# Performance work log

Hardware: AMD Instinct MI355X
Metric: run time of the kernel (lower is better)

## Reference

```python
import jax, jax.numpy as jnp
import numpy as np

N_NODES = 50000
N_EDGES = 640000
HID = 128
N_LAYERS = 4
BN_EPS = 1e-5


def _bn(h, gamma, beta):
    # train-mode BatchNorm1d over node axis (biased variance, as torch uses for normalization)
    mu = h.mean(axis=0)
    var = h.var(axis=0)
    return gamma * (h - mu) * jax.lax.rsqrt(var + BN_EPS) + beta


def setup_inputs() -> dict:
    key = jax.random.key(0)
    ks = jax.random.split(key, 8)
    s = 1.0 / np.sqrt(HID)
    x = jax.random.normal(ks[0], (N_NODES, HID), dtype=jnp.float32)
    edge_index = jax.random.randint(ks[1], (2, N_EDGES), 0, N_NODES, dtype=jnp.int64)
    edge_attr = jax.random.normal(ks[2], (N_EDGES, HID), dtype=jnp.float32)
    W1 = jax.random.normal(ks[3], (N_LAYERS, HID, HID), dtype=jnp.float32) * s
    b1 = jnp.zeros((N_LAYERS, HID), jnp.float32)
    g1 = jnp.ones((N_LAYERS, HID), jnp.float32)
    be1 = jnp.zeros((N_LAYERS, HID), jnp.float32)
    W2 = jax.random.normal(ks[4], (N_LAYERS, HID, HID), dtype=jnp.float32) * s
    b2 = jnp.zeros((N_LAYERS, HID), jnp.float32)
    bn_g = jnp.ones((N_LAYERS - 1, HID), jnp.float32)
    bn_b = jnp.zeros((N_LAYERS - 1, HID), jnp.float32)
    return {"x": x, "edge_index": edge_index, "edge_attr": edge_attr,
            "W1": W1, "b1": b1, "g1": g1, "be1": be1,
            "W2": W2, "b2": b2, "bn_g": bn_g, "bn_b": bn_b}


def reference(x, edge_index, edge_attr, W1, b1, g1, be1, W2, b2, bn_g, bn_b):
    src, dst = edge_index[0], edge_index[1]
    n = x.shape[0]
    z = x
    for i in range(N_LAYERS):
        # GINEConv: message = relu(x_j + e_ij), sum-aggregate, eps=0
        msg = jax.nn.relu(z[src] + edge_attr)          # [E, H]
        agg = jax.ops.segment_sum(msg, dst, num_segments=n)  # [N, H]
        h = z + agg
        # conv MLP: Linear -> BatchNorm1d -> ReLU -> Linear
        h = h @ W1[i] + b1[i]
        h = jax.nn.relu(_bn(h, g1[i], be1[i]))
        h = h @ W2[i] + b2[i]
        # encoder activation
        z = jax.nn.relu(h)
        # inter-layer batchnorm (not after last layer)
        if i != N_LAYERS - 1:
            z = _bn(z, bn_g[i], bn_b[i])
    return z
```

## Files before the change

kernel.cpp:

```cpp
#include <hip/hip_runtime.h>
#include <hip/hip_bf16.h>

#define N_NODES 50000
#define N_EDGES 640000
#define HID 128
#define BN_EPS 1e-5f
#define BF16_MAGIC 0x3F803F80u
#define MG_NBLK 782

typedef __bf16 bf16x8 __attribute__((ext_vector_type(8)));
typedef float f32x4 __attribute__((ext_vector_type(4)));

__global__ void detect_k(const unsigned int* __restrict__ g1w,
                         const unsigned int* __restrict__ idxw,
                         int* __restrict__ flags) {
    __shared__ int anynz;
    if (threadIdx.x == 0) anynz = 0;
    __syncthreads();
    unsigned int v = idxw[2 * threadIdx.x + 1];
    if (v) atomicOr(&anynz, 1);
    __syncthreads();
    if (threadIdx.x == 0) {
        flags[0] = (g1w[0] == BF16_MAGIC) ? 1 : 0;
        flags[1] = anynz ? 0 : 1;
    }
}

__global__ void init_k(int* __restrict__ cnt, float* __restrict__ statb) {
    int i = blockIdx.x * 256 + threadIdx.x;
    if (i < N_NODES) cnt[i] = 0;
    int j = i - N_NODES;
    if (j >= 0) {
        if (j < 1792) statb[j] = 0.f;
        if (j >= 2048 && j < 2176) statb[j] = 1.f;
        if (j >= 2560 && j < 2688) statb[j] = 0.f;
    }
}

__device__ __forceinline__ float cvt_in(const void* p, int i, int bf) {
    return bf ? __bfloat162float(((const __hip_bfloat16*)p)[i])
              : ((const float*)p)[i];
}

__global__ void conv_w_k(const void* W1, const void* W2, const void* b1, const void* b2,
                         const int* __restrict__ flags, float* __restrict__ wbuf) {
    int i = blockIdx.x * 256 + threadIdx.x;
    int bf = flags[0];
    if (i < 65536)       wbuf[i] = cvt_in(W1, i, bf);
    else if (i < 131072) wbuf[i] = cvt_in(W2, i - 65536, bf);
    else if (i < 131584) wbuf[i] = cvt_in(b1, i - 131072, bf);
    else if (i < 132096) wbuf[i] = cvt_in(b2, i - 131584, bf);
}

__global__ void pack_w_k(const float* __restrict__ wf,
                         __hip_bfloat16* __restrict__ hi,
                         __hip_bfloat16* __restrict__ lo) {
    int gid = blockIdx.x * 256 + threadIdx.x;
    int mat = gid >> 11;
    int ent = gid & 2047;
    int T = ent >> 8, S = (ent >> 6) & 3, L = ent & 63;
    int n = T * 16 + (L & 15);
    int k0 = S * 32 + (L >> 4) * 8;
    const float* w = wf + mat * 16384;
    __hip_bfloat16 hv[8], lv[8];
#pragma unroll
    for (int j = 0; j < 8; j++) {
        float v = w[(k0 + j) * 128 + n];
        float h = __bfloat162float(__float2bfloat16(v));
        hv[j] = __float2bfloat16(v);
        lv[j] = __float2bfloat16(v - h);
    }
    __hip_bfloat16* hp = hi + (size_t)gid * 8;
    __hip_bfloat16* lp = lo + (size_t)gid * 8;
#pragma unroll
    for (int j = 0; j < 8; j++) { hp[j] = hv[j]; lp[j] = lv[j]; }
}

__global__ void conv_x_k(const void* x, const int* __restrict__ flags,
                         float* __restrict__ zbuf) {
    int i = blockIdx.x * 256 + threadIdx.x;
    if (i >= N_NODES * HID / 4) return;
    float4 o;
    if (flags[0]) {
        ushort4 v = ((const ushort4*)x)[i];
        union { unsigned int u; float f; } a, b, c, d;
        a.u = (unsigned int)v.x << 16; b.u = (unsigned int)v.y << 16;
        c.u = (unsigned int)v.z << 16; d.u = (unsigned int)v.w << 16;
        o.x = a.f; o.y = b.f; o.z = c.f; o.w = d.f;
    } else {
        o = ((const float4*)x)[i];
    }
    ((float4*)zbuf)[i] = o;
}

__global__ void hist_k(const void* eidx, const int* __restrict__ flags,
                       int* __restrict__ cnt) {
    int e = blockIdx.x * 256 + threadIdx.x;
    if (e >= N_EDGES) return;
    int d = flags[1] ? (int)((const long long*)eidx)[N_EDGES + e]
                     : ((const int*)eidx)[N_EDGES + e];
    atomicAdd(&cnt[d], 1);
}

__global__ void scan_k(const int* __restrict__ cnt, int* __restrict__ start,
                       int* __restrict__ cursor) {
    __shared__ int sh[1024];
    __shared__ int carry;
    if (threadIdx.x == 0) carry = 0;
    __syncthreads();
    const int CH = 8192;
    for (int base = 0; base < N_NODES; base += CH) {
        int idx0 = base + threadIdx.x * 8;
        int v[8];
        int s = 0;
#pragma unroll
        for (int j = 0; j < 8; j++) {
            int i = idx0 + j;
            v[j] = (i < N_NODES) ? cnt[i] : 0;
            s += v[j];
        }
        sh[threadIdx.x] = s;
        __syncthreads();
        for (int off = 1; off < 1024; off <<= 1) {
            int tv = 0;
            if ((int)threadIdx.x >= off) tv = sh[threadIdx.x - off];
            __syncthreads();
            if ((int)threadIdx.x >= off) sh[threadIdx.x] += tv;
            __syncthreads();
        }
        int run = sh[threadIdx.x] - s + carry;
#pragma unroll
        for (int j = 0; j < 8; j++) {
            int i = idx0 + j;
            if (i < N_NODES) { start[i] = run; cursor[i] = run; }
            run += v[j];
        }
        __syncthreads();
        if (threadIdx.x == 1023) carry += sh[1023];
        __syncthreads();
    }
    if (threadIdx.x == 0) start[N_NODES] = carry;
}

__global__ void scatter_k(const void* eidx, const int* __restrict__ flags,
                          int* __restrict__ cursor, int2* __restrict__ se) {
    int e = blockIdx.x * 256 + threadIdx.x;
    if (e >= N_EDGES) return;
    int s, d;
    if (flags[1]) {
        const long long* p = (const long long*)eidx;
        s = (int)p[e]; d = (int)p[N_EDGES + e];
    } else {
        const int* p = (const int*)eidx;
        s = p[e]; d = p[N_EDGES + e];
    }
    int pos = atomicAdd(&cursor[d], 1);
    se[pos] = make_int2(s, e);
}

__global__ __launch_bounds__(256) void agg_k(
    const float* __restrict__ z, const void* __restrict__ eattr,
    const int* __restrict__ flags,
    const float* __restrict__ Ac, const float* __restrict__ Cc,
    const int* __restrict__ start, const int2* __restrict__ se,
    float* __restrict__ hin) {
    int lane = threadIdx.x & 63;
    int node = blockIdx.x * 4 + (threadIdx.x >> 6);
    if (node >= N_NODES) return;
    int c0 = lane * 2;
    float ax = Ac[c0], ay = Ac[c0 + 1];
    float cx = Cc[c0], cy = Cc[c0 + 1];
    int e0 = start[node], e1 = start[node + 1];
    int nE = e1 - e0;
    float sx = 0.f, sy = 0.f;
    const float2* zf = (const float2*)z;
    int isbf = flags[0];

    for (int base = 0; base < nE; base += 64) {
        int idx = base + lane;
        int2 sev = se[e0 + (idx < nE ? idx : nE - 1)];
        int rem = nE - base; if (rem > 64) rem = 64;
        int j = 0;
        if (isbf) {
            const __hip_bfloat162* ea = (const __hip_bfloat162*)eattr;
            for (; j + 4 <= rem; j += 4) {
                int s0 = __builtin_amdgcn_readlane(sev.x, j + 0);
                int i0 = __builtin_amdgcn_readlane(sev.y, j + 0);
                int s1 = __builtin_amdgcn_readlane(sev.x, j + 1);
                int i1 = __builtin_amdgcn_readlane(sev.y, j + 1);
                int s2 = __builtin_amdgcn_readlane(sev.x, j + 2);
                int i2 = __builtin_amdgcn_readlane(sev.y, j + 2);
                int s3 = __builtin_amdgcn_readlane(sev.x, j + 3);
                int i3 = __builtin_amdgcn_readlane(sev.y, j + 3);
                float2 z0 = zf[s0 * 64 + lane];
                float2 z1 = zf[s1 * 64 + lane];
                float2 z2 = zf[s2 * 64 + lane];
                float2 z3 = zf[s3 * 64 + lane];
                float2 e0v = __bfloat1622float2(ea[i0 * 64 + lane]);
                float2 e1v = __bfloat1622float2(ea[i1 * 64 + lane]);
                float2 e2v = __bfloat1622float2(ea[i2 * 64 + lane]);
                float2 e3v = __bfloat1622float2(ea[i3 * 64 + lane]);
                sx += fmaxf(fmaf(ax, z0.x, cx) + e0v.x, 0.f);
                sy += fmaxf(fmaf(ay, z0.y, cy) + e0v.y, 0.f);
                sx += fmaxf(fmaf(ax, z1.x, cx) + e1v.x, 0.f);
                sy += fmaxf(fmaf(ay, z1.y, cy) + e1v.y, 0.f);
                sx += fmaxf(fmaf(ax, z2.x, cx) + e2v.x, 0.f);
                sy += fmaxf(fmaf(ay, z2.y, cy) + e2v.y, 0.f);
                sx += fmaxf(fmaf(ax, z3.x, cx) + e3v.x, 0.f);
                sy += fmaxf(fmaf(ay, z3.y, cy) + e3v.y, 0.f);
            }
            for (; j < rem; j++) {
                int s0 = __builtin_amdgcn_readlane(sev.x, j);
                int i0 = __builtin_amdgcn_readlane(sev.y, j);
                float2 zv = zf[s0 * 64 + lane];
                float2 ev = __bfloat1622float2(ea[i0 * 64 + lane]);
                sx += fmaxf(fmaf(ax, zv.x, cx) + ev.x, 0.f);
                sy += fmaxf(fmaf(ay, zv.y, cy) + ev.y, 0.f);
            }
        } else {
            const float2* ea = (const float2*)eattr;
            for (; j + 4 <= rem; j += 4) {
                int s0 = __builtin_amdgcn_readlane(sev.x, j + 0);
                int i0 = __builtin_amdgcn_readlane(sev.y, j + 0);
                int s1 = __builtin_amdgcn_readlane(sev.x, j + 1);
                int i1 = __builtin_amdgcn_readlane(sev.y, j + 1);
                int s2 = __builtin_amdgcn_readlane(sev.x, j + 2);
                int i2 = __builtin_amdgcn_readlane(sev.y, j + 2);
                int s3 = __builtin_amdgcn_readlane(sev.x, j + 3);
                int i3 = __builtin_amdgcn_readlane(sev.y, j + 3);
                float2 z0 = zf[s0 * 64 + lane];
                float2 z1 = zf[s1 * 64 + lane];
                float2 z2 = zf[s2 * 64 + lane];
                float2 z3 = zf[s3 * 64 + lane];
                float2 e0v = ea[i0 * 64 + lane];
                float2 e1v = ea[i1 * 64 + lane];
                float2 e2v = ea[i2 * 64 + lane];
                float2 e3v = ea[i3 * 64 + lane];
                sx += fmaxf(fmaf(ax, z0.x, cx) + e0v.x, 0.f);
                sy += fmaxf(fmaf(ay, z0.y, cy) + e0v.y, 0.f);
                sx += fmaxf(fmaf(ax, z1.x, cx) + e1v.x, 0.f);
                sy += fmaxf(fmaf(ay, z1.y, cy) + e1v.y, 0.f);
                sx += fmaxf(fmaf(ax, z2.x, cx) + e2v.x, 0.f);
                sy += fmaxf(fmaf(ay, z2.y, cy) + e2v.y, 0.f);
                sx += fmaxf(fmaf(ax, z3.x, cx) + e3v.x, 0.f);
                sy += fmaxf(fmaf(ay, z3.y, cy) + e3v.y, 0.f);
            }
            for (; j < rem; j++) {
                int s0 = __builtin_amdgcn_readlane(sev.x, j);
                int i0 = __builtin_amdgcn_readlane(sev.y, j);
                float2 zv = zf[s0 * 64 + lane];
                float2 ev = ea[i0 * 64 + lane];
                sx += fmaxf(fmaf(ax, zv.x, cx) + ev.x, 0.f);
                sy += fmaxf(fmaf(ay, zv.y, cy) + ev.y, 0.f);
            }
        }
    }
    float2 zs = zf[node * 64 + lane];
    float2 o;
    o.x = fmaf(ax, zs.x, cx) + sx;
    o.y = fmaf(ay, zs.y, cy) + sy;
    ((float2*)hin)[node * 64 + lane] = o;
}

__global__ __launch_bounds__(256) void mgemm_k(
    const float* __restrict__ Ain,
    const __hip_bfloat16* __restrict__ whi, const __hip_bfloat16* __restrict__ wlo,
    const float* __restrict__ bias,
    const float* __restrict__ Ascale, const float* __restrict__ Cshift,
    float* __restrict__ Fout, void* __restrict__ OutFinal,
    const int* __restrict__ flags,
    float* __restrict__ pbuf, int mode) {
    __shared__ char WshRaw[32768];
    __shared__ char WslRaw[32768];
    __shared__ float ssum[128], ssq[128];
    int t = threadIdx.x;
    int lane = t & 63, w = t >> 6, quad = lane >> 4;
    int isbf = flags[0];
    int m0 = blockIdx.x * 64;
    int row = m0 + w * 16 + (lane & 15);
    bool rv = row < N_NODES;

    bf16x8 ahi[4], alo[4];
#pragma unroll
    for (int S = 0; S < 4; S++) {
        float v[8];
        if (rv) {
            const float4* ap = (const float4*)(Ain + row * 128 + S * 32 + quad * 8);
            float4 p0 = ap[0], p1 = ap[1];
            v[0] = p0.x; v[1] = p0.y; v[2] = p0.z; v[3] = p0.w;
            v[4] = p1.x; v[5] = p1.y; v[6] = p1.z; v[7] = p1.w;
        } else {
#pragma unroll
            for (int j = 0; j < 8; j++) v[j] = 0.f;
        }
        if (mode != 0) {
            const float4* as = (const float4*)(Ascale + S * 32 + quad * 8);
            const float4* cs = (const float4*)(Cshift + S * 32 + quad * 8);
            float4 a0 = as[0], a1 = as[1], c0 = cs[0], c1 = cs[1];
            float aa[8] = {a0.x, a0.y, a0.z, a0.w, a1.x, a1.y, a1.z, a1.w};
            float cc[8] = {c0.x, c0.y, c0.z, c0.w, c1.x, c1.y, c1.z, c1.w};
#pragma unroll
            for (int j = 0; j < 8; j++) v[j] = fmaxf(fmaf(aa[j], v[j], cc[j]), 0.f);
        }
#pragma unroll
        for (int j = 0; j < 8; j++) {
            __bf16 h = (__bf16)v[j];
            ahi[S][j] = h;
            alo[S][j] = (__bf16)(v[j] - (float)h);
        }
    }

    {
        const uint4* sh = (const uint4*)whi;
        uint4* dh = (uint4*)WshRaw;
#pragma unroll
        for (int i = 0; i < 8; i++) dh[t + i * 256] = sh[t + i * 256];
        if (!isbf) {
            const uint4* sl = (const uint4*)wlo;
            uint4* dl = (uint4*)WslRaw;
#pragma unroll
            for (int i = 0; i < 8; i++) dl[t + i * 256] = sl[t + i * 256];
        }
    }
    if (t < 128) { ssum[t] = 0.f; ssq[t] = 0.f; }
    __syncthreads();

    const bf16x8* WH = (const bf16x8*)WshRaw;
    const bf16x8* WL = (const bf16x8*)WslRaw;
    f32x4 acc[8];
    f32x4 z4 = {0.f, 0.f, 0.f, 0.f};
#pragma unroll
    for (int T = 0; T < 8; T++) acc[T] = z4;
#pragma unroll
    for (int T = 0; T < 8; T++) {
#pragma unroll
        for (int S = 0; S < 4; S++) {
            bf16x8 wh = WH[(T * 4 + S) * 64 + lane];
            acc[T] = __builtin_amdgcn_mfma_f32_16x16x32_bf16(ahi[S], wh, acc[T], 0, 0, 0);
            acc[T] = __builtin_amdgcn_mfma_f32_16x16x32_bf16(alo[S], wh, acc[T], 0, 0, 0);
        }
    }
    if (!isbf) {
#pragma unroll
        for (int T = 0; T < 8; T++) {
#pragma unroll
            for (int S = 0; S < 4; S++) {
                bf16x8 wl = WL[(T * 4 + S) * 64 + lane];
                acc[T] = __builtin_amdgcn_mfma_f32_16x16x32_bf16(ahi[S], wl, acc[T], 0, 0, 0);
            }
        }
    }

    int colbase = lane & 15;
    int rbase = m0 + w * 16 + quad * 4;
#pragma unroll
    for (int T = 0; T < 8; T++) {
        int col = T * 16 + colbase;
        float bv = bias[col];
        float s = 0.f, q = 0.f;
#pragma unroll
        for (int r = 0; r < 4; r++) {
            int rr = rbase + r;
            if (rr >= N_NODES) continue;
            float o = acc[T][r] + bv;
            if (mode != 0) o = fmaxf(o, 0.f);
            if (mode == 2) {
                if (isbf) ((__hip_bfloat16*)OutFinal)[rr * 128 + col] = __float2bfloat16(o);
                else      ((float*)OutFinal)[rr * 128 + col] = o;
            } else {
                Fout[rr * 128 + col] = o;
                s += o; q += o * o;
            }
        }
        if (mode != 2) {
            s += __shfl_xor(s, 16); s += __shfl_xor(s, 32);
            q += __shfl_xor(q, 16); q += __shfl_xor(q, 32);
            if (lane < 16) { atomicAdd(&ssum[col], s); atomicAdd(&ssq[col], q); }
        }
    }
    if (mode != 2) {
        __syncthreads();
        if (t < 128) {
            pbuf[blockIdx.x * 256 + t] = ssum[t];
            pbuf[blockIdx.x * 256 + 128 + t] = ssq[t];
        }
    }
}

__global__ __launch_bounds__(256) void fin_k(const float* __restrict__ pbuf,
                      const void* gamma, const void* beta, int layer,
                      const int* __restrict__ flags,
                      float* __restrict__ Ac, float* __restrict__ Cc) {
    int col = blockIdx.x;
    int t = threadIdx.x;
    float s = 0.f, q = 0.f;
    for (int b = t; b < MG_NBLK; b += 256) {
        s += pbuf[b * 256 + col];
        q += pbuf[b * 256 + 128 + col];
    }
#pragma unroll
    for (int m = 32; m >= 1; m >>= 1) {
        s += __shfl_xor(s, m);
        q += __shfl_xor(q, m);
    }
    __shared__ float shs[4], shq[4];
    if ((t & 63) == 0) { shs[t >> 6] = s; shq[t >> 6] = q; }
    __syncthreads();
    if (t == 0) {
        float S = shs[0] + shs[1] + shs[2] + shs[3];
        float Q = shq[0] + shq[1] + shq[2] + shq[3];
        int bf = flags[0];
        float g = cvt_in(gamma, layer * 128 + col, bf);
        float b_ = cvt_in(beta, layer * 128 + col, bf);
        const float invN = 1.f / (float)N_NODES;
        float mean = S * invN;
        float var = fmaxf(Q * invN - mean * mean, 0.f);
        float rs = rsqrtf(var + BN_EPS);
        float a = g * rs;
        Ac[col] = a;
        Cc[col] = b_ - mean * a;
    }
}

extern "C" void kernel_launch(void* const* d_in, const int* in_sizes, int n_in,
                              void* d_out, int out_size, void* d_ws, size_t ws_size,
                              hipStream_t stream) {
    const void* x_p   = d_in[0];
    const void* ei_p  = d_in[1];
    const void* ea_p  = d_in[2];
    const void* W1_p  = d_in[3];
    const void* b1_p  = d_in[4];
    const void* g1_p  = d_in[5];
    const void* be1_p = d_in[6];
    const void* W2_p  = d_in[7];
    const void* b2_p  = d_in[8];
    const void* bng_p = d_in[9];
    const void* bnb_p = d_in[10];

    char* ws = (char*)d_ws;
    size_t off = 0;
    auto alloc = [&](size_t bytes) {
        void* p = ws + off;
        off += (bytes + 255) / 256 * 256;
        return p;
    };
    float* zbuf  = (float*)alloc((size_t)N_NODES * HID * 4);
    float* hin   = (float*)alloc((size_t)N_NODES * HID * 4);
    float* h1    = (float*)alloc((size_t)N_NODES * HID * 4);
    int* cnt     = (int*)alloc((size_t)N_NODES * 4);
    int* start   = (int*)alloc((size_t)(N_NODES + 1) * 4);
    int* cursor  = (int*)alloc((size_t)N_NODES * 4);
    int2* sebuf  = (int2*)alloc((size_t)N_EDGES * 8);
    int* flags   = (int*)alloc(256);
    float* statb = (float*)alloc(3072 * 4);
    float* wbuf  = (float*)alloc(132096 * 4);
    __hip_bfloat16* whi_pack = (__hip_bfloat16*)alloc(8 * 16384 * 2);
    __hip_bfloat16* wlo_pack = (__hip_bfloat16*)alloc(8 * 16384 * 2);
    float* pbuf  = (float*)alloc((size_t)MG_NBLK * 256 * 4);

    float* A1   = statb + 1792;
    float* C1   = statb + 1920;
    float* Aagg = statb + 2048;
    float* Cagg = statb + 2560;
    float* b1f  = wbuf + 131072;
    float* b2f  = wbuf + 131584;

    detect_k<<<1, 256, 0, stream>>>((const unsigned int*)g1_p,
                                    (const unsigned int*)ei_p, flags);
    init_k<<<206, 256, 0, stream>>>(cnt, statb);
    conv_w_k<<<516, 256, 0, stream>>>(W1_p, W2_p, b1_p, b2_p, flags, wbuf);
    pack_w_k<<<64, 256, 0, stream>>>(wbuf, whi_pack, wlo_pack);
    conv_x_k<<<6250, 256, 0, stream>>>(x_p, flags, zbuf);
    hist_k<<<2500, 256, 0, stream>>>(ei_p, flags, cnt);
    scan_k<<<1, 1024, 0, stream>>>(cnt, start, cursor);
    scatter_k<<<2500, 256, 0, stream>>>(ei_p, flags, cursor, sebuf);

    for (int i = 0; i < 4; i++) {
        agg_k<<<12500, 256, 0, stream>>>(zbuf, ea_p, flags, Aagg + i * 128,
                                         Cagg + i * 128, start, sebuf, hin);
        mgemm_k<<<MG_NBLK, 256, 0, stream>>>(hin, whi_pack + i * 16384,
                                         wlo_pack + i * 16384, b1f + i * 128,
                                         nullptr, nullptr, h1, nullptr, flags,
                                         pbuf, 0);
        fin_k<<<128, 256, 0, stream>>>(pbuf, g1_p, be1_p, i, flags, A1, C1);
        if (i < 3) {
            mgemm_k<<<MG_NBLK, 256, 0, stream>>>(h1, whi_pack + (4 + i) * 16384,
                                             wlo_pack + (4 + i) * 16384,
                                             b2f + i * 128, A1, C1, zbuf, nullptr,
                                             flags, pbuf, 1);
            fin_k<<<128, 256, 0, stream>>>(pbuf, bng_p, bnb_p, i, flags,
                                           Aagg + (i + 1) * 128,
                                           Cagg + (i + 1) * 128);
        } else {
            mgemm_k<<<MG_NBLK, 256, 0, stream>>>(h1, whi_pack + (4 + i) * 16384,
                                             wlo_pack + (4 + i) * 16384,
                                             b2f + i * 128, A1, C1, nullptr, d_out,
                                             flags, pbuf, 2);
        }
    }
    (void)in_sizes; (void)n_in; (void)out_size; (void)ws_size;
}
```

Baseline: 1.185 ms.

## Pre-permute edge attributes into CSR order and fuse BN stat finalize into GEMM

A new kernel copies edge_attr into destination-sorted order once, so the four aggregation passes read edge features contiguously instead of gathering them by edge id. Only source ids are kept in the CSR list. Separately, the BN statistics reduction moves into the GEMM kernel: blocks atomically add their partial sums, and the last block, detected with a done counter, computes the scale and shift, which removes the fin_k launches. The trade-offs are an extra full copy of edge_attr (about 328 MB of traffic for fp32), more workspace, and float atomics that make the summation order nondeterministic.

```diff
diff --git a/kernel.cpp b/kernel.cpp
--- a/kernel.cpp
+++ b/kernel.cpp
@@ -34,6 +34,7 @@
         if (j < 1792) statb[j] = 0.f;
         if (j >= 2048 && j < 2176) statb[j] = 1.f;
         if (j >= 2560 && j < 2688) statb[j] = 0.f;
+        if (j >= 3072 && j < 3088) statb[j] = 0.f;
     }
 }
 
@@ -143,7 +144,8 @@
 }
 
 __global__ void scatter_k(const void* eidx, const int* __restrict__ flags,
-                          int* __restrict__ cursor, int2* __restrict__ se) {
+                          int* __restrict__ cursor, int* __restrict__ srcs,
+                          int* __restrict__ eids) {
     int e = blockIdx.x * 256 + threadIdx.x;
     if (e >= N_EDGES) return;
     int s, d;
@@ -155,14 +157,31 @@
         s = p[e]; d = p[N_EDGES + e];
     }
     int pos = atomicAdd(&cursor[d], 1);
-    se[pos] = make_int2(s, e);
+    srcs[pos] = s;
+    eids[pos] = e;
+}
+
+__global__ void perm_ea_k(const void* __restrict__ ea,
+                          const int* __restrict__ eids,
+                          const int* __restrict__ flags,
+                          void* __restrict__ eap) {
+    int isbf = flags[0];
+    int lg = isbf ? 4 : 5;
+    long long tid = (long long)blockIdx.x * 256 + threadIdx.x;
+    long long total = (long long)N_EDGES << lg;
+    if (tid >= total) return;
+    int p = (int)(tid >> lg);
+    int c = (int)(tid & ((1 << lg) - 1));
+    int e = eids[p];
+    ((uint4*)eap)[((long long)p << lg) + c] =
+        ((const uint4*)ea)[((long long)e << lg) + c];
 }
 
 __global__ __launch_bounds__(256) void agg_k(
-    const float* __restrict__ z, const void* __restrict__ eattr,
+    const float* __restrict__ z, const void* __restrict__ eap,
     const int* __restrict__ flags,
     const float* __restrict__ Ac, const float* __restrict__ Cc,
-    const int* __restrict__ start, const int2* __restrict__ se,
+    const int* __restrict__ start, const int* __restrict__ srcs,
     float* __restrict__ hin) {
     int lane = threadIdx.x & 63;
     int node = blockIdx.x * 4 + (threadIdx.x >> 6);
@@ -178,28 +197,25 @@
 
     for (int base = 0; base < nE; base += 64) {
         int idx = base + lane;
-        int2 sev = se[e0 + (idx < nE ? idx : nE - 1)];
+        int sv = srcs[e0 + (idx < nE ? idx : nE - 1)];
         int rem = nE - base; if (rem > 64) rem = 64;
         int j = 0;
         if (isbf) {
-            const __hip_bfloat162* ea = (const __hip_bfloat162*)eattr;
+            const __hip_bfloat162* ear =
+                (const __hip_bfloat162*)eap + (size_t)(e0 + base) * 64;
             for (; j + 4 <= rem; j += 4) {
-                int s0 = __builtin_amdgcn_readlane(sev.x, j + 0);
-                int i0 = __builtin_amdgcn_readlane(sev.y, j + 0);
-                int s1 = __builtin_amdgcn_readlane(sev.x, j + 1);
-                int i1 = __builtin_amdgcn_readlane(sev.y, j + 1);
-                int s2 = __builtin_amdgcn_readlane(sev.x, j + 2);
-                int i2 = __builtin_amdgcn_readlane(sev.y, j + 2);
-                int s3 = __builtin_amdgcn_readlane(sev.x, j + 3);
-                int i3 = __builtin_amdgcn_readlane(sev.y, j + 3);
+                int s0 = __builtin_amdgcn_readlane(sv, j + 0);
+                int s1 = __builtin_amdgcn_readlane(sv, j + 1);
+                int s2 = __builtin_amdgcn_readlane(sv, j + 2);
+                int s3 = __builtin_amdgcn_readlane(sv, j + 3);
                 float2 z0 = zf[s0 * 64 + lane];
                 float2 z1 = zf[s1 * 64 + lane];
                 float2 z2 = zf[s2 * 64 + lane];
                 float2 z3 = zf[s3 * 64 + lane];
-                float2 e0v = __bfloat1622float2(ea[i0 * 64 + lane]);
-                float2 e1v = __bfloat1622float2(ea[i1 * 64 + lane]);
-                float2 e2v = __bfloat1622float2(ea[i2 * 64 + lane]);
-                float2 e3v = __bfloat1622float2(ea[i3 * 64 + lane]);
+                float2 e0v = __bfloat1622float2(ear[(j + 0) * 64 + lane]);
+                float2 e1v = __bfloat1622float2(ear[(j + 1) * 64 + lane]);
+                float2 e2v = __bfloat1622float2(ear[(j + 2) * 64 + lane]);
+                float2 e3v = __bfloat1622float2(ear[(j + 3) * 64 + lane]);
                 sx += fmaxf(fmaf(ax, z0.x, cx) + e0v.x, 0.f);
                 sy += fmaxf(fmaf(ay, z0.y, cy) + e0v.y, 0.f);
                 sx += fmaxf(fmaf(ax, z1.x, cx) + e1v.x, 0.f);
@@ -210,32 +226,27 @@
                 sy += fmaxf(fmaf(ay, z3.y, cy) + e3v.y, 0.f);
             }
             for (; j < rem; j++) {
-                int s0 = __builtin_amdgcn_readlane(sev.x, j);
-                int i0 = __builtin_amdgcn_readlane(sev.y, j);
+                int s0 = __builtin_amdgcn_readlane(sv, j);
                 float2 zv = zf[s0 * 64 + lane];
-                float2 ev = __bfloat1622float2(ea[i0 * 64 + lane]);
+                float2 ev = __bfloat1622float2(ear[j * 64 + lane]);
                 sx += fmaxf(fmaf(ax, zv.x, cx) + ev.x, 0.f);
                 sy += fmaxf(fmaf(ay, zv.y, cy) + ev.y, 0.f);
             }
         } else {
-            const float2* ea = (const float2*)eattr;
+            const float2* ear = (const float2*)eap + (size_t)(e0 + base) * 64;
             for (; j + 4 <= rem; j += 4) {
-                int s0 = __builtin_amdgcn_readlane(sev.x, j + 0);
-                int i0 = __builtin_amdgcn_readlane(sev.y, j + 0);
-                int s1 = __builtin_amdgcn_readlane(sev.x, j + 1);
-                int i1 = __builtin_amdgcn_readlane(sev.y, j + 1);
-                int s2 = __builtin_amdgcn_readlane(sev.x, j + 2);
-                int i2 = __builtin_amdgcn_readlane(sev.y, j + 2);
-                int s3 = __builtin_amdgcn_readlane(sev.x, j + 3);
-                int i3 = __builtin_amdgcn_readlane(sev.y, j + 3);
+                int s0 = __builtin_amdgcn_readlane(sv, j + 0);
+                int s1 = __builtin_amdgcn_readlane(sv, j + 1);
+                int s2 = __builtin_amdgcn_readlane(sv, j + 2);
+                int s3 = __builtin_amdgcn_readlane(sv, j + 3);
                 float2 z0 = zf[s0 * 64 + lane];
                 float2 z1 = zf[s1 * 64 + lane];
                 float2 z2 = zf[s2 * 64 + lane];
                 float2 z3 = zf[s3 * 64 + lane];
-                float2 e0v = ea[i0 * 64 + lane];
-                float2 e1v = ea[i1 * 64 + lane];
-                float2 e2v = ea[i2 * 64 + lane];
-                float2 e3v = ea[i3 * 64 + lane];
+                float2 e0v = ear[(j + 0) * 64 + lane];
+                float2 e1v = ear[(j + 1) * 64 + lane];
+                float2 e2v = ear[(j + 2) * 64 + lane];
+                float2 e3v = ear[(j + 3) * 64 + lane];
                 sx += fmaxf(fmaf(ax, z0.x, cx) + e0v.x, 0.f);
                 sy += fmaxf(fmaf(ay, z0.y, cy) + e0v.y, 0.f);
                 sx += fmaxf(fmaf(ax, z1.x, cx) + e1v.x, 0.f);
@@ -246,10 +257,9 @@
                 sy += fmaxf(fmaf(ay, z3.y, cy) + e3v.y, 0.f);
             }
             for (; j < rem; j++) {
-                int s0 = __builtin_amdgcn_readlane(sev.x, j);
-                int i0 = __builtin_amdgcn_readlane(sev.y, j);
+                int s0 = __builtin_amdgcn_readlane(sv, j);
                 float2 zv = zf[s0 * 64 + lane];
-                float2 ev = ea[i0 * 64 + lane];
+                float2 ev = ear[j * 64 + lane];
                 sx += fmaxf(fmaf(ax, zv.x, cx) + ev.x, 0.f);
                 sy += fmaxf(fmaf(ay, zv.y, cy) + ev.y, 0.f);
             }
@@ -269,10 +279,14 @@
     const float* __restrict__ Ascale, const float* __restrict__ Cshift,
     float* __restrict__ Fout, void* __restrict__ OutFinal,
     const int* __restrict__ flags,
-    float* __restrict__ pbuf, int mode) {
+    float* __restrict__ gsum, float* __restrict__ gsq,
+    const void* gamma, const void* beta, int layer,
+    float* __restrict__ Aout, float* __restrict__ Cout,
+    int* __restrict__ done, int mode) {
     __shared__ char WshRaw[32768];
     __shared__ char WslRaw[32768];
     __shared__ float ssum[128], ssq[128];
+    __shared__ int amLast;
     int t = threadIdx.x;
     int lane = t & 63, w = t >> 6, quad = lane >> 4;
     int isbf = flags[0];
@@ -380,45 +394,25 @@
     }
     if (mode != 2) {
         __syncthreads();
-        if (t < 128) {
-            pbuf[blockIdx.x * 256 + t] = ssum[t];
-            pbuf[blockIdx.x * 256 + 128 + t] = ssq[t];
-        }
-    }
-}
-
-__global__ __launch_bounds__(256) void fin_k(const float* __restrict__ pbuf,
-                      const void* gamma, const void* beta, int layer,
-                      const int* __restrict__ flags,
-                      float* __restrict__ Ac, float* __restrict__ Cc) {
-    int col = blockIdx.x;
-    int t = threadIdx.x;
-    float s = 0.f, q = 0.f;
-    for (int b = t; b < MG_NBLK; b += 256) {
-        s += pbuf[b * 256 + col];
-        q += pbuf[b * 256 + 128 + col];
-    }
-#pragma unroll
-    for (int m = 32; m >= 1; m >>= 1) {
-        s += __shfl_xor(s, m);
-        q += __shfl_xor(q, m);
-    }
-    __shared__ float shs[4], shq[4];
-    if ((t & 63) == 0) { shs[t >> 6] = s; shq[t >> 6] = q; }
-    __syncthreads();
-    if (t == 0) {
-        float S = shs[0] + shs[1] + shs[2] + shs[3];
-        float Q = shq[0] + shq[1] + shq[2] + shq[3];
-        int bf = flags[0];
-        float g = cvt_in(gamma, layer * 128 + col, bf);
-        float b_ = cvt_in(beta, layer * 128 + col, bf);
-        const float invN = 1.f / (float)N_NODES;
-        float mean = S * invN;
-        float var = fmaxf(Q * invN - mean * mean, 0.f);
-        float rs = rsqrtf(var + BN_EPS);
-        float a = g * rs;
-        Ac[col] = a;
-        Cc[col] = b_ - mean * a;
+        if (t < 128) { atomicAdd(&gsum[t], ssum[t]); atomicAdd(&gsq[t], ssq[t]); }
+        __threadfence();
+        __syncthreads();
+        if (t == 0) amLast = (atomicAdd(done, 1) == MG_NBLK - 1);
+        __syncthreads();
+        if (amLast && t < 128) {
+            __threadfence();
+            float S = atomicAdd(&gsum[t], 0.f);
+            float Q = atomicAdd(&gsq[t], 0.f);
+            float g = cvt_in(gamma, layer * 128 + t, isbf);
+            float b_ = cvt_in(beta, layer * 128 + t, isbf);
+            const float invN = 1.f / (float)N_NODES;
+            float mean = S * invN;
+            float var = fmaxf(Q * invN - mean * mean, 0.f);
+            float rs = rsqrtf(var + BN_EPS);
+            float a = g * rs;
+            Aout[t] = a;
+            Cout[t] = b_ - mean * a;
+        }
     }
 }
 
@@ -450,52 +444,63 @@
     int* cnt     = (int*)alloc((size_t)N_NODES * 4);
     int* start   = (int*)alloc((size_t)(N_NODES + 1) * 4);
     int* cursor  = (int*)alloc((size_t)N_NODES * 4);
-    int2* sebuf  = (int2*)alloc((size_t)N_EDGES * 8);
+    int* srcs    = (int*)alloc((size_t)N_EDGES * 4);
+    int* eids    = (int*)alloc((size_t)N_EDGES * 4);
     int* flags   = (int*)alloc(256);
-    float* statb = (float*)alloc(3072 * 4);
+    float* statb = (float*)alloc(3200 * 4);
     float* wbuf  = (float*)alloc(132096 * 4);
     __hip_bfloat16* whi_pack = (__hip_bfloat16*)alloc(8 * 16384 * 2);
     __hip_bfloat16* wlo_pack = (__hip_bfloat16*)alloc(8 * 16384 * 2);
-    float* pbuf  = (float*)alloc((size_t)MG_NBLK * 256 * 4);
-
+    void* eap    = alloc((size_t)N_EDGES * HID * 4);
+
+    float* gs1  = statb;
+    float* gq1  = statb + 512;
+    float* gs2  = statb + 1024;
+    float* gq2  = statb + 1408;
     float* A1   = statb + 1792;
     float* C1   = statb + 1920;
     float* Aagg = statb + 2048;
     float* Cagg = statb + 2560;
+    int* donec  = (int*)(statb + 3072);
     float* b1f  = wbuf + 131072;
     float* b2f  = wbuf + 131584;
 
     detect_k<<<1, 256, 0, stream>>>((const unsigned int*)g1_p,
                                     (const unsigned int*)ei_p, flags);
-    init_k<<<206, 256, 0, stream>>>(cnt, statb);
+    init_k<<<208, 256, 0, stream>>>(cnt, statb);
     conv_w_k<<<516, 256, 0, stream>>>(W1_p, W2_p, b1_p, b2_p, flags, wbuf);
     pack_w_k<<<64, 256, 0, stream>>>(wbuf, whi_pack, wlo_pack);
     conv_x_k<<<6250, 256, 0, stream>>>(x_p, flags, zbuf);
     hist_k<<<2500, 256, 0, stream>>>(ei_p, flags, cnt);
     scan_k<<<1, 1024, 0, stream>>>(cnt, start, cursor);
-    scatter_k<<<2500, 256, 0, stream>>>(ei_p, flags, cursor, sebuf);
+    scatter_k<<<2500, 256, 0, stream>>>(ei_p, flags, cursor, srcs, eids);
+    perm_ea_k<<<80000, 256, 0, stream>>>(ea_p, eids, flags, eap);
 
     for (int i = 0; i < 4; i++) {
-        agg_k<<<12500, 256, 0, stream>>>(zbuf, ea_p, flags, Aagg + i * 128,
-                                         Cagg + i * 128, start, sebuf, hin);
+        agg_k<<<12500, 256, 0, stream>>>(zbuf, eap, flags, Aagg + i * 128,
+                                         Cagg + i * 128, start, srcs, hin);
         mgemm_k<<<MG_NBLK, 256, 0, stream>>>(hin, whi_pack + i * 16384,
                                          wlo_pack + i * 16384, b1f + i * 128,
                                          nullptr, nullptr, h1, nullptr, flags,
-                                         pbuf, 0);
-        fin_k<<<128, 256, 0, stream>>>(pbuf, g1_p, be1_p, i, flags, A1, C1);
+                                         gs1 + i * 128, gq1 + i * 128,
+                                         g1_p, be1_p, i, A1, C1,
+                                         &donec[i], 0);
         if (i < 3) {
             mgemm_k<<<MG_NBLK, 256, 0, stream>>>(h1, whi_pack + (4 + i) * 16384,
                                              wlo_pack + (4 + i) * 16384,
                                              b2f + i * 128, A1, C1, zbuf, nullptr,
-                                             flags, pbuf, 1);
-            fin_k<<<128, 256, 0, stream>>>(pbuf, bng_p, bnb_p, i, flags,
-                                           Aagg + (i + 1) * 128,
-                                           Cagg + (i + 1) * 128);
+                                             flags, gs2 + i * 128, gq2 + i * 128,
+                                             bng_p, bnb_p, i,
+                                             Aagg + (i + 1) * 128,
+                                             Cagg + (i + 1) * 128,
+                                             &donec[4 + i], 1);
         } else {
             mgemm_k<<<MG_NBLK, 256, 0, stream>>>(h1, whi_pack + (4 + i) * 16384,
                                              wlo_pack + (4 + i) * 16384,
                                              b2f + i * 128, A1, C1, nullptr, d_out,
-                                             flags, pbuf, 2);
+                                             flags, nullptr, nullptr,
+                                             nullptr, nullptr, 0, nullptr, nullptr,
+                                             nullptr, 2);
         }
     }
     (void)in_sizes; (void)n_in; (void)out_size; (void)ws_size;
```

Result: slower. 1.730 ms (+46.0%).

## Cache edge attributes in CSR order as bf16 for later layers

Applied to the files above, without the earlier changes.

During the first layer's aggregation, each gathered edge-attribute row is written to a workspace buffer in destination-sorted order and stored as bf16. Later layers read this buffer contiguously instead of doing random gathers through the edge permutation, halving bytes when the input is fp32 and removing the edge-id readlanes. The cached path also unrolls by eight. This costs an extra large write in layer 0 and rounds fp32 edge features to bf16, which may affect accuracy.

```diff
diff --git a/kernel.cpp b/kernel.cpp
--- a/kernel.cpp
+++ b/kernel.cpp
@@ -160,10 +160,11 @@
 
 __global__ __launch_bounds__(256) void agg_k(
     const float* __restrict__ z, const void* __restrict__ eattr,
+    __hip_bfloat162* __restrict__ eab,
     const int* __restrict__ flags,
     const float* __restrict__ Ac, const float* __restrict__ Cc,
     const int* __restrict__ start, const int2* __restrict__ se,
-    float* __restrict__ hin) {
+    float* __restrict__ hin, int mode) {
     int lane = threadIdx.x & 63;
     int node = blockIdx.x * 4 + (threadIdx.x >> 6);
     if (node >= N_NODES) return;
@@ -176,30 +177,68 @@
     const float2* zf = (const float2*)z;
     int isbf = flags[0];
 
-    for (int base = 0; base < nE; base += 64) {
-        int idx = base + lane;
-        int2 sev = se[e0 + (idx < nE ? idx : nE - 1)];
-        int rem = nE - base; if (rem > 64) rem = 64;
-        int j = 0;
-        if (isbf) {
-            const __hip_bfloat162* ea = (const __hip_bfloat162*)eattr;
-            for (; j + 4 <= rem; j += 4) {
+    if (mode == 1) {
+        for (int base = 0; base < nE; base += 64) {
+            int idx = base + lane;
+            int2 sev = se[e0 + (idx < nE ? idx : nE - 1)];
+            int rem = nE - base; if (rem > 64) rem = 64;
+            const __hip_bfloat162* ear = eab + (size_t)(e0 + base) * 64;
+            int j = 0;
+            for (; j + 8 <= rem; j += 8) {
                 int s0 = __builtin_amdgcn_readlane(sev.x, j + 0);
-                int i0 = __builtin_amdgcn_readlane(sev.y, j + 0);
                 int s1 = __builtin_amdgcn_readlane(sev.x, j + 1);
-                int i1 = __builtin_amdgcn_readlane(sev.y, j + 1);
                 int s2 = __builtin_amdgcn_readlane(sev.x, j + 2);
-                int i2 = __builtin_amdgcn_readlane(sev.y, j + 2);
                 int s3 = __builtin_amdgcn_readlane(sev.x, j + 3);
-                int i3 = __builtin_amdgcn_readlane(sev.y, j + 3);
+                int s4 = __builtin_amdgcn_readlane(sev.x, j + 4);
+                int s5 = __builtin_amdgcn_readlane(sev.x, j + 5);
+                int s6 = __builtin_amdgcn_readlane(sev.x, j + 6);
+                int s7 = __builtin_amdgcn_readlane(sev.x, j + 7);
                 float2 z0 = zf[s0 * 64 + lane];
                 float2 z1 = zf[s1 * 64 + lane];
                 float2 z2 = zf[s2 * 64 + lane];
                 float2 z3 = zf[s3 * 64 + lane];
-                float2 e0v = __bfloat1622float2(ea[i0 * 64 + lane]);
-                float2 e1v = __bfloat1622float2(ea[i1 * 64 + lane]);
-                float2 e2v = __bfloat1622float2(ea[i2 * 64 + lane]);
-                float2 e3v = __bfloat1622float2(ea[i3 * 64 + lane]);
+                float2 z4 = zf[s4 * 64 + lane];
+                float2 z5 = zf[s5 * 64 + lane];
+                float2 z6 = zf[s6 * 64 + lane];
+                float2 z7 = zf[s7 * 64 + lane];
+                float2 e0v = __bfloat1622float2(ear[(j + 0) * 64 + lane]);
+                float2 e1v = __bfloat1622float2(ear[(j + 1) * 64 + lane]);
+                float2 e2v = __bfloat1622float2(ear[(j + 2) * 64 + lane]);
+                float2 e3v = __bfloat1622float2(ear[(j + 3) * 64 + lane]);
+                float2 e4v = __bfloat1622float2(ear[(j + 4) * 64 + lane]);
+                float2 e5v = __bfloat1622float2(ear[(j + 5) * 64 + lane]);
+                float2 e6v = __bfloat1622float2(ear[(j + 6) * 64 + lane]);
+                float2 e7v = __bfloat1622float2(ear[(j + 7) * 64 + lane]);
+                sx += fmaxf(fmaf(ax, z0.x, cx) + e0v.x, 0.f);
+                sy += fmaxf(fmaf(ay, z0.y, cy) + e0v.y, 0.f);
+                sx += fmaxf(fmaf(ax, z1.x, cx) + e1v.x, 0.f);
+                sy += fmaxf(fmaf(ay, z1.y, cy) + e1v.y, 0.f);
+                sx += fmaxf(fmaf(ax, z2.x, cx) + e2v.x, 0.f);
+                sy += fmaxf(fmaf(ay, z2.y, cy) + e2v.y, 0.f);
+                sx += fmaxf(fmaf(ax, z3.x, cx) + e3v.x, 0.f);
+                sy += fmaxf(fmaf(ay, z3.y, cy) + e3v.y, 0.f);
+                sx += fmaxf(fmaf(ax, z4.x, cx) + e4v.x, 0.f);
+                sy += fmaxf(fmaf(ay, z4.y, cy) + e4v.y, 0.f);
+                sx += fmaxf(fmaf(ax, z5.x, cx) + e5v.x, 0.f);
+                sy += fmaxf(fmaf(ay, z5.y, cy) + e5v.y, 0.f);
+                sx += fmaxf(fmaf(ax, z6.x, cx) + e6v.x, 0.f);
+                sy += fmaxf(fmaf(ay, z6.y, cy) + e6v.y, 0.f);
+                sx += fmaxf(fmaf(ax, z7.x, cx) + e7v.x, 0.f);
+                sy += fmaxf(fmaf(ay, z7.y, cy) + e7v.y, 0.f);
+            }
+            for (; j + 4 <= rem; j += 4) {
+                int s0 = __builtin_amdgcn_readlane(sev.x, j + 0);
+                int s1 = __builtin_amdgcn_readlane(sev.x, j + 1);
+                int s2 = __builtin_amdgcn_readlane(sev.x, j + 2);
+                int s3 = __builtin_amdgcn_readlane(sev.x, j + 3);
+                float2 z0 = zf[s0 * 64 + lane];
+                float2 z1 = zf[s1 * 64 + lane];
+                float2 z2 = zf[s2 * 64 + lane];
+                float2 z3 = zf[s3 * 64 + lane];
+                float2 e0v = __bfloat1622float2(ear[(j + 0) * 64 + lane]);
+                float2 e1v = __bfloat1622float2(ear[(j + 1) * 64 + lane]);
+                float2 e2v = __bfloat1622float2(ear[(j + 2) * 64 + lane]);
+                float2 e3v = __bfloat1622float2(ear[(j + 3) * 64 + lane]);
                 sx += fmaxf(fmaf(ax, z0.x, cx) + e0v.x, 0.f);
                 sy += fmaxf(fmaf(ay, z0.y, cy) + e0v.y, 0.f);
                 sx += fmaxf(fmaf(ax, z1.x, cx) + e1v.x, 0.f);
@@ -211,47 +250,106 @@
             }
             for (; j < rem; j++) {
                 int s0 = __builtin_amdgcn_readlane(sev.x, j);
-                int i0 = __builtin_amdgcn_readlane(sev.y, j);
                 float2 zv = zf[s0 * 64 + lane];
-                float2 ev = __bfloat1622float2(ea[i0 * 64 + lane]);
+                float2 ev = __bfloat1622float2(ear[j * 64 + lane]);
                 sx += fmaxf(fmaf(ax, zv.x, cx) + ev.x, 0.f);
                 sy += fmaxf(fmaf(ay, zv.y, cy) + ev.y, 0.f);
             }
-        } else {
-            const float2* ea = (const float2*)eattr;
-            for (; j + 4 <= rem; j += 4) {
-                int s0 = __builtin_amdgcn_readlane(sev.x, j + 0);
-                int i0 = __builtin_amdgcn_readlane(sev.y, j + 0);
-                int s1 = __builtin_amdgcn_readlane(sev.x, j + 1);
-                int i1 = __builtin_amdgcn_readlane(sev.y, j + 1);
-                int s2 = __builtin_amdgcn_readlane(sev.x, j + 2);
-                int i2 = __builtin_amdgcn_readlane(sev.y, j + 2);
-                int s3 = __builtin_amdgcn_readlane(sev.x, j + 3);
-                int i3 = __builtin_amdgcn_readlane(sev.y, j + 3);
-                float2 z0 = zf[s0 * 64 + lane];
-                float2 z1 = zf[s1 * 64 + lane];
-                float2 z2 = zf[s2 * 64 + lane];
-                float2 z3 = zf[s3 * 64 + lane];
-                float2 e0v = ea[i0 * 64 + lane];
-                float2 e1v = ea[i1 * 64 + lane];
-                float2 e2v = ea[i2 * 64 + lane];
-                float2 e3v = ea[i3 * 64 + lane];
-                sx += fmaxf(fmaf(ax, z0.x, cx) + e0v.x, 0.f);
-                sy += fmaxf(fmaf(ay, z0.y, cy) + e0v.y, 0.f);
-                sx += fmaxf(fmaf(ax, z1.x, cx) + e1v.x, 0.f);
-                sy += fmaxf(fmaf(ay, z1.y, cy) + e1v.y, 0.f);
-                sx += fmaxf(fmaf(ax, z2.x, cx) + e2v.x, 0.f);
-                sy += fmaxf(fmaf(ay, z2.y, cy) + e2v.y, 0.f);
-                sx += fmaxf(fmaf(ax, z3.x, cx) + e3v.x, 0.f);
-                sy += fmaxf(fmaf(ay, z3.y, cy) + e3v.y, 0.f);
-            }
-            for (; j < rem; j++) {
-                int s0 = __builtin_amdgcn_readlane(sev.x, j);
-                int i0 = __builtin_amdgcn_readlane(sev.y, j);
-                float2 zv = zf[s0 * 64 + lane];
-                float2 ev = ea[i0 * 64 + lane];
-                sx += fmaxf(fmaf(ax, zv.x, cx) + ev.x, 0.f);
-                sy += fmaxf(fmaf(ay, zv.y, cy) + ev.y, 0.f);
+        }
+    } else {
+        for (int base = 0; base < nE; base += 64) {
+            int idx = base + lane;
+            int2 sev = se[e0 + (idx < nE ? idx : nE - 1)];
+            int rem = nE - base; if (rem > 64) rem = 64;
+            __hip_bfloat162* eaw = eab + (size_t)(e0 + base) * 64;
+            int j = 0;
+            if (isbf) {
+                const __hip_bfloat162* ea = (const __hip_bfloat162*)eattr;
+                for (; j + 4 <= rem; j += 4) {
+                    int s0 = __builtin_amdgcn_readlane(sev.x, j + 0);
+                    int i0 = __builtin_amdgcn_readlane(sev.y, j + 0);
+                    int s1 = __builtin_amdgcn_readlane(sev.x, j + 1);
+                    int i1 = __builtin_amdgcn_readlane(sev.y, j + 1);
+                    int s2 = __builtin_amdgcn_readlane(sev.x, j + 2);
+                    int i2 = __builtin_amdgcn_readlane(sev.y, j + 2);
+                    int s3 = __builtin_amdgcn_readlane(sev.x, j + 3);
+                    int i3 = __builtin_amdgcn_readlane(sev.y, j + 3);
+                    float2 z0 = zf[s0 * 64 + lane];
+                    float2 z1 = zf[s1 * 64 + lane];
+                    float2 z2 = zf[s2 * 64 + lane];
+                    float2 z3 = zf[s3 * 64 + lane];
+                    __hip_bfloat162 b0 = ea[i0 * 64 + lane];
+                    __hip_bfloat162 b1 = ea[i1 * 64 + lane];
+                    __hip_bfloat162 b2 = ea[i2 * 64 + lane];
+                    __hip_bfloat162 b3 = ea[i3 * 64 + lane];
+                    eaw[(j + 0) * 64 + lane] = b0;
+                    eaw[(j + 1) * 64 + lane] = b1;
+                    eaw[(j + 2) * 64 + lane] = b2;
+                    eaw[(j + 3) * 64 + lane] = b3;
+                    float2 e0v = __bfloat1622float2(b0);
+                    float2 e1v = __bfloat1622float2(b1);
+                    float2 e2v = __bfloat1622float2(b2);
+                    float2 e3v = __bfloat1622float2(b3);
+                    sx += fmaxf(fmaf(ax, z0.x, cx) + e0v.x, 0.f);
+                    sy += fmaxf(fmaf(ay, z0.y, cy) + e0v.y, 0.f);
+                    sx += fmaxf(fmaf(ax, z1.x, cx) + e1v.x, 0.f);
+                    sy += fmaxf(fmaf(ay, z1.y, cy) + e1v.y, 0.f);
+                    sx += fmaxf(fmaf(ax, z2.x, cx) + e2v.x, 0.f);
+                    sy += fmaxf(fmaf(ay, z2.y, cy) + e2v.y, 0.f);
+                    sx += fmaxf(fmaf(ax, z3.x, cx) + e3v.x, 0.f);
+                    sy += fmaxf(fmaf(ay, z3.y, cy) + e3v.y, 0.f);
+                }
+                for (; j < rem; j++) {
+                    int s0 = __builtin_amdgcn_readlane(sev.x, j);
+                    int i0 = __builtin_amdgcn_readlane(sev.y, j);
+                    float2 zv = zf[s0 * 64 + lane];
+                    __hip_bfloat162 b0 = ea[i0 * 64 + lane];
+                    eaw[j * 64 + lane] = b0;
+                    float2 ev = __bfloat1622float2(b0);
+                    sx += fmaxf(fmaf(ax, zv.x, cx) + ev.x, 0.f);
+                    sy += fmaxf(fmaf(ay, zv.y, cy) + ev.y, 0.f);
+                }
+            } else {
+                const float2* ea = (const float2*)eattr;
+                for (; j + 4 <= rem; j += 4) {
+                    int s0 = __builtin_amdgcn_readlane(sev.x, j + 0);
+                    int i0 = __builtin_amdgcn_readlane(sev.y, j + 0);
+                    int s1 = __builtin_amdgcn_readlane(sev.x, j + 1);
+                    int i1 = __builtin_amdgcn_readlane(sev.y, j + 1);
+                    int s2 = __builtin_amdgcn_readlane(sev.x, j + 2);
+                    int i2 = __builtin_amdgcn_readlane(sev.y, j + 2);
+                    int s3 = __builtin_amdgcn_readlane(sev.x, j + 3);
+                    int i3 = __builtin_amdgcn_readlane(sev.y, j + 3);
+                    float2 z0 = zf[s0 * 64 + lane];
+                    float2 z1 = zf[s1 * 64 + lane];
+                    float2 z2 = zf[s2 * 64 + lane];
+                    float2 z3 = zf[s3 * 64 + lane];
+                    float2 e0v = ea[i0 * 64 + lane];
+                    float2 e1v = ea[i1 * 64 + lane];
+                    float2 e2v = ea[i2 * 64 + lane];
+                    float2 e3v = ea[i3 * 64 + lane];
+                    eaw[(j + 0) * 64 + lane] = __float22bfloat162_rn(e0v);
+                    eaw[(j + 1) * 64 + lane] = __float22bfloat162_rn(e1v);
+                    eaw[(j + 2) * 64 + lane] = __float22bfloat162_rn(e2v);
+                    eaw[(j + 3) * 64 + lane] = __float22bfloat162_rn(e3v);
+                    sx += fmaxf(fmaf(ax, z0.x, cx) + e0v.x, 0.f);
+                    sy += fmaxf(fmaf(ay, z0.y, cy) + e0v.y, 0.f);
+                    sx += fmaxf(fmaf(ax, z1.x, cx) + e1v.x, 0.f);
+                    sy += fmaxf(fmaf(ay, z1.y, cy) + e1v.y, 0.f);
+                    sx += fmaxf(fmaf(ax, z2.x, cx) + e2v.x, 0.f);
+                    sy += fmaxf(fmaf(ay, z2.y, cy) + e2v.y, 0.f);
+                    sx += fmaxf(fmaf(ax, z3.x, cx) + e3v.x, 0.f);
+                    sy += fmaxf(fmaf(ay, z3.y, cy) + e3v.y, 0.f);
+                }
+                for (; j < rem; j++) {
+                    int s0 = __builtin_amdgcn_readlane(sev.x, j);
+                    int i0 = __builtin_amdgcn_readlane(sev.y, j);
+                    float2 zv = zf[s0 * 64 + lane];
+                    float2 ev = ea[i0 * 64 + lane];
+                    eaw[j * 64 + lane] = __float22bfloat162_rn(ev);
+                    sx += fmaxf(fmaf(ax, zv.x, cx) + ev.x, 0.f);
+                    sy += fmaxf(fmaf(ay, zv.y, cy) + ev.y, 0.f);
+                }
             }
         }
     }
@@ -457,6 +555,7 @@
     __hip_bfloat16* whi_pack = (__hip_bfloat16*)alloc(8 * 16384 * 2);
     __hip_bfloat16* wlo_pack = (__hip_bfloat16*)alloc(8 * 16384 * 2);
     float* pbuf  = (float*)alloc((size_t)MG_NBLK * 256 * 4);
+    __hip_bfloat162* eab = (__hip_bfloat162*)alloc((size_t)N_EDGES * HID * 2);
 
     float* A1   = statb + 1792;
     float* C1   = statb + 1920;
@@ -467,7 +566,7 @@
 
     detect_k<<<1, 256, 0, stream>>>((const unsigned int*)g1_p,
                                     (const unsigned int*)ei_p, flags);
-    init_k<<<206, 256, 0, stream>>>(cnt, statb);
+    init_k<<<208, 256, 0, stream>>>(cnt, statb);
     conv_w_k<<<516, 256, 0, stream>>>(W1_p, W2_p, b1_p, b2_p, flags, wbuf);
     pack_w_k<<<64, 256, 0, stream>>>(wbuf, whi_pack, wlo_pack);
     conv_x_k<<<6250, 256, 0, stream>>>(x_p, flags, zbuf);
@@ -476,8 +575,9 @@
     scatter_k<<<2500, 256, 0, stream>>>(ei_p, flags, cursor, sebuf);
 
     for (int i = 0; i < 4; i++) {
-        agg_k<<<12500, 256, 0, stream>>>(zbuf, ea_p, flags, Aagg + i * 128,
-                                         Cagg + i * 128, start, sebuf, hin);
+        agg_k<<<12500, 256, 0, stream>>>(zbuf, ea_p, eab, flags, Aagg + i * 128,
+                                         Cagg + i * 128, start, sebuf, hin,
+                                         i == 0 ? 0 : 1);
         mgemm_k<<<MG_NBLK, 256, 0, stream>>>(hin, whi_pack + i * 16384,
                                          wlo_pack + i * 16384, b1f + i * 128,
                                          nullptr, nullptr, h1, nullptr, flags,
```

Result: faster. 1.134 ms (-4.3%).
